# Optimization experiments

Measured on AMD Instinct MI355X. Metric: run time of the kernel, lower is better.

## Reference

```python
import jax, jax.numpy as jnp
import numpy as np

B, G, A, C = 32, 2704, 3, 6
D, H, W = 1024, 52, 52
L, HID, K = 20, 512, 128


def setup_inputs() -> dict:
    key = jax.random.key(0)
    ks = jax.random.split(key, 7)
    return {
        "boxes": jax.random.normal(ks[0], (B, G, A, C), dtype=jnp.float32),
        "feature": jax.random.normal(ks[1], (B, D, H, W), dtype=jnp.float32),
        "text": jax.random.normal(ks[2], (B, L, HID), dtype=jnp.float32),
        "W_vs": jax.random.normal(ks[3], (D, HID), dtype=jnp.float32) * 0.02,
        "b_vs": jax.random.normal(ks[4], (HID,), dtype=jnp.float32) * 0.02,
        "W_tx": jax.random.normal(ks[5], (HID, HID), dtype=jnp.float32) * 0.02,
        "b_tx": jax.random.normal(ks[6], (HID,), dtype=jnp.float32) * 0.02,
        "select_num": K,
    }


def reference(boxes, feature, text, W_vs, b_vs, W_tx, b_tx, select_num):
    # objectness score: mean over anchors, channel 4  -> [B, G]
    score = jnp.mean(boxes, axis=2)[:, :, 4]
    _, idx = jax.lax.top_k(score, select_num)          # [B, K]
    # torch path builds a boolean mask then masked_select, which keeps
    # selected cells in grid order -> sort indices ascending
    idx = jnp.sort(idx, axis=1)

    # gather selected boxes: [B, K, A, C]
    sel_boxes = jnp.take_along_axis(boxes, idx[:, :, None, None], axis=1)

    b, d, h, w = feature.shape
    feat = feature.reshape(b, d, h * w).transpose(0, 2, 1)  # [B, G, D]
    sel_feat = jnp.take_along_axis(feat, idx[:, :, None], axis=1)  # [B, K, D]

    linear_feature = sel_feat @ W_vs + b_vs   # [B, K, HID]
    linear_text = text @ W_tx + b_tx          # [B, L, HID]

    # pack head inputs into a single array for baseline comparison
    out = jnp.concatenate([linear_feature, linear_text], axis=1)  # [B, K+L, HID]
    return out, sel_boxes
```

## Files before the change

kernel.cpp:

```cpp
#include <hip/hip_runtime.h>
#include <cstddef>

namespace {
constexpr int cB = 32;
constexpr int cG = 2704;
constexpr int cA = 3;
constexpr int cC = 6;
constexpr int cD = 1024;
constexpr int cL = 20;
constexpr int cH = 512;
constexpr int cK = 128;
constexpr int ROWS_OUT = cK + cL;
constexpr int FTHREADS = 512;
constexpr int CHUNK = (cG + FTHREADS - 1) / FTHREADS;
}

using u16x8 = __attribute__((ext_vector_type(8))) unsigned short;
using f32x4 = __attribute__((ext_vector_type(4))) float;
using bf16x8 = __attribute__((ext_vector_type(8))) short;

static __device__ __forceinline__ unsigned short f2bf(float f) {
  unsigned u = __float_as_uint(f);
  unsigned rounding = 0x7fffu + ((u >> 16) & 1u);
  return (unsigned short)((u + rounding) >> 16);
}
static __device__ __forceinline__ unsigned packbf(float lo, float hi) {
  return (unsigned)f2bf(lo) | ((unsigned)f2bf(hi) << 16);
}

__global__ __launch_bounds__(FTHREADS) void front_kernel(
    const float* __restrict__ boxes, const float* __restrict__ W_vs,
    const float* __restrict__ W_tx, const float* __restrict__ text,
    int* __restrict__ idx_out, float* __restrict__ out_boxes,
    unsigned short* __restrict__ Wt_vs, unsigned short* __restrict__ Wt_tx,
    unsigned short* __restrict__ text_bf) {
  __shared__ unsigned su[cG];
  __shared__ int hist[256];
  __shared__ int wsum[8];
  __shared__ int ssel[cK];
  __shared__ int s_rem;
  __shared__ unsigned s_prefix;
  __shared__ float tile[64][65];

  const int tid = threadIdx.x;
  const int lane = tid & 63;
  const int wv = tid >> 6;

  if (blockIdx.x < cB) {
    const int b = blockIdx.x;
    for (int g = tid; g < cG; g += FTHREADS) {
      const float* p = boxes + ((size_t)(b * cG + g) * cA) * cC + 4;
      float s = (p[0] + p[cC] + p[2 * cC]) * (1.0f / 3.0f);
      unsigned bits = __float_as_uint(s);
      su[g] = (bits & 0x80000000u) ? ~bits : (bits | 0x80000000u);
    }
    __syncthreads();

    int remaining = cK;
    unsigned prefix = 0;
    for (int pass = 0; pass < 4; ++pass) {
      const int shift = 24 - 8 * pass;
      if (tid < 256) hist[tid] = 0;
      __syncthreads();
      for (int g = tid; g < cG; g += FTHREADS) {
        unsigned u = su[g];
        if ((pass == 0) || ((u >> (shift + 8)) == (prefix >> (shift + 8))))
          atomicAdd(&hist[(u >> shift) & 255], 1);
      }
      __syncthreads();
      if (tid < 256) {
        int h = hist[tid];
        int x = h;
#pragma unroll
        for (int d = 1; d < 64; d <<= 1) {
          int n = __shfl_up(x, d);
          if (lane >= d) x += n;
        }
        if (lane == 63) wsum[wv] = x;
        __syncthreads();
        int off = 0, T = 0;
#pragma unroll
        for (int w = 0; w < 4; ++w) {
          int s = wsum[w];
          T += s;
          if (w < wv) off += s;
        }
        const int pincl = x + off;
        const int pexcl = pincl - h;
        const int target = T - remaining;
        if (target >= pexcl && target < pincl) {
          s_prefix = prefix | ((unsigned)tid << shift);
          s_rem = remaining - (T - pincl);
        }
      } else {
        __syncthreads();
      }
      __syncthreads();
      remaining = s_rem;
      prefix = s_prefix;
    }

    const int g0 = tid * CHUNK;
    const int g1 = min(g0 + CHUNK, cG);
    int cgt = 0, ceq = 0;
    for (int g = g0; g < g1; ++g) {
      unsigned u = su[g];
      cgt += (u > prefix);
      ceq += (u == prefix);
    }
    int packed = (cgt << 16) | ceq;
    int x = packed;
#pragma unroll
    for (int d = 1; d < 64; d <<= 1) {
      int n = __shfl_up(x, d);
      if (lane >= d) x += n;
    }
    if (lane == 63) wsum[wv] = x;
    __syncthreads();
    int off = 0;
#pragma unroll
    for (int w = 0; w < 8; ++w)
      if (w < wv) off += wsum[w];
    const int excl = x + off - packed;
    int gt_before = excl >> 16;
    int eq_before = excl & 0xffff;

    for (int g = g0; g < g1; ++g) {
      unsigned u = su[g];
      if (u > prefix) {
        ssel[gt_before + min(eq_before, remaining)] = g;
        ++gt_before;
      } else if (u == prefix) {
        if (eq_before < remaining) ssel[gt_before + eq_before] = g;
        ++eq_before;
      }
    }
    __syncthreads();

    if (tid < cK) idx_out[b * cK + tid] = ssel[tid];
    for (int t2 = tid; t2 < cK * (cA * cC); t2 += FTHREADS) {
      const int k = t2 / 18;
      const int e = t2 - k * 18;
      out_boxes[(size_t)(b * cK + k) * 18 + e] =
          boxes[((size_t)(b * cG) + ssel[k]) * 18 + e];
    }
  } else {
    const int t = blockIdx.x - cB;
    if (t < 128) {
      const int k0 = (t >> 3) * 64, n0 = (t & 7) * 64;
      for (int i = tid; i < 1024; i += FTHREADS) {
        const int kk = i >> 4, c4 = (i & 15) * 4;
        const float4 v =
            *(const float4*)(W_vs + (size_t)(k0 + kk) * cH + n0 + c4);
        tile[kk][c4 + 0] = v.x;
        tile[kk][c4 + 1] = v.y;
        tile[kk][c4 + 2] = v.z;
        tile[kk][c4 + 3] = v.w;
      }
      __syncthreads();
      for (int j = tid; j < 2048; j += FTHREADS) {
        const int nn = j >> 5, p = j & 31;
        unsigned v = packbf(tile[2 * p][nn], tile[2 * p + 1][nn]);
        *(unsigned*)(Wt_vs + (size_t)(n0 + nn) * cD + k0 + 2 * p) = v;
      }
    } else if (t < 192) {
      const int t2 = t - 128;
      const int k0 = (t2 >> 3) * 64, n0 = (t2 & 7) * 64;
      for (int i = tid; i < 1024; i += FTHREADS) {
        const int kk = i >> 4, c4 = (i & 15) * 4;
        const float4 v =
            *(const float4*)(W_tx + (size_t)(k0 + kk) * cH + n0 + c4);
        tile[kk][c4 + 0] = v.x;
        tile[kk][c4 + 1] = v.y;
        tile[kk][c4 + 2] = v.z;
        tile[kk][c4 + 3] = v.w;
      }
      __syncthreads();
      for (int j = tid; j < 2048; j += FTHREADS) {
        const int nn = j >> 5, p = j & 31;
        unsigned v = packbf(tile[2 * p][nn], tile[2 * p + 1][nn]);
        *(unsigned*)(Wt_tx + (size_t)(n0 + nn) * cH + k0 + 2 * p) = v;
      }
    } else {
      const int t3 = t - 192;
      const size_t base = (size_t)t3 * 4096;
      for (int i = tid; i < 1024; i += FTHREADS) {
        const float4 v = *(const float4*)(text + base + (size_t)i * 4);
        uint2 pv;
        pv.x = packbf(v.x, v.y);
        pv.y = packbf(v.z, v.w);
        *(uint2*)(text_bf + base + (size_t)i * 4) = pv;
      }
    }
  }
}

__global__ __launch_bounds__(256) void gather_feat_kernel(
    const float* __restrict__ feature, const int* __restrict__ idx,
    unsigned short* __restrict__ selfeat) {
  const int kc = blockIdx.x;
  const int dc = blockIdx.y;
  const int b = blockIdx.z;
  const int tid = threadIdx.x;
  const int lane = tid & 63;
  const int grp = tid >> 6;
  __shared__ int sidx[64];
  __shared__ float tile[32][65];
  if (tid < 64) sidx[tid] = idx[b * cK + kc * 64 + tid];
  __syncthreads();

  const int g = sidx[lane];
  const float* fptr =
      feature + (size_t)b * cD * cG + (size_t)(dc * 32 + grp * 8) * cG + g;
  float f[8];
#pragma unroll
  for (int j = 0; j < 8; ++j) f[j] = __builtin_nontemporal_load(fptr + (size_t)j * cG);
#pragma unroll
  for (int j = 0; j < 8; ++j) tile[grp * 8 + j][lane] = f[j];
  __syncthreads();

  const size_t obase = ((size_t)(b * cK + kc * 64)) * cD + dc * 32;
#pragma unroll
  for (int it = 0; it < 2; ++it) {
    const int i = tid + it * 256;
    const int kk = i >> 3;
    const int q = i & 7;
    uint2 pv;
    pv.x = packbf(tile[4 * q + 0][kk], tile[4 * q + 1][kk]);
    pv.y = packbf(tile[4 * q + 2][kk], tile[4 * q + 3][kk]);
    *(uint2*)(selfeat + obase + (size_t)kk * cD + 4 * q) = pv;
  }
}

template <int KD>
__device__ __forceinline__ void mfma_gemm_body(
    const unsigned short* __restrict__ A, const unsigned short* __restrict__ Bt,
    const float* __restrict__ bias, float* __restrict__ out, int bm, int bn,
    int rpb, int row_off, unsigned short (*As)[128][40],
    unsigned short (*Bs)[128][40]) {
  constexpr int NT = KD / 32;
  const int tid = threadIdx.x;
  const int wid = tid >> 6, lane = tid & 63;
  const int wr = wid >> 2, wc = wid & 3;
  const int lr = lane & 15, lg = lane >> 4;

  const int srow = tid >> 2;
  const int sc = (tid & 3) * 8;

  const unsigned short* pA = A + (size_t)(bm * 128 + srow) * KD + sc;
  const unsigned short* pB = Bt + (size_t)(bn * 128 + srow) * KD + sc;

  f32x4 acc[4][2];
#pragma unroll
  for (int i = 0; i < 4; ++i)
#pragma unroll
    for (int j = 0; j < 2; ++j) acc[i][j] = {0.f, 0.f, 0.f, 0.f};

  u16x8 xa, xb;
  u16x8 ya, yb;

#define LOAD_X(kt)                      \
  xa = *(const u16x8*)(pA + (kt) * 32); \
  xb = *(const u16x8*)(pB + (kt) * 32);
#define LOAD_Y(kt)                      \
  ya = *(const u16x8*)(pA + (kt) * 32); \
  yb = *(const u16x8*)(pB + (kt) * 32);
#define STORE_X(buf)                \
  *(u16x8*)&As[buf][srow][sc] = xa; \
  *(u16x8*)&Bs[buf][srow][sc] = xb;
#define STORE_Y(buf)                \
  *(u16x8*)&As[buf][srow][sc] = ya; \
  *(u16x8*)&Bs[buf][srow][sc] = yb;
#define COMPUTE(buf)                                                        \
  {                                                                         \
    bf16x8 af[4], bfr[2];                                                   \
    _Pragma("unroll") for (int fr = 0; fr < 4; ++fr) af[fr] =               \
        *(const bf16x8*)&As[buf][wr * 64 + fr * 16 + lr][lg * 8];           \
    _Pragma("unroll") for (int fc = 0; fc < 2; ++fc) bfr[fc] =              \
        *(const bf16x8*)&Bs[buf][wc * 32 + fc * 16 + lr][lg * 8];           \
    _Pragma("unroll") for (int fr = 0; fr < 4; ++fr)                        \
        _Pragma("unroll") for (int fc = 0; fc < 2; ++fc) acc[fr][fc] =      \
            __builtin_amdgcn_mfma_f32_16x16x32_bf16(af[fr], bfr[fc],        \
                                                    acc[fr][fc], 0, 0, 0);  \
  }

  LOAD_X(0);
  LOAD_Y(1);
  STORE_X(0);
  __syncthreads();

  for (int t = 0; t < NT; t += 2) {
    if (t + 2 < NT) LOAD_X(t + 2);
    COMPUTE(0);
    STORE_Y(1);
    __syncthreads();
    if (t + 3 < NT) LOAD_Y(t + 3);
    COMPUTE(1);
    if (t + 2 < NT) STORE_X(0);
    __syncthreads();
  }
#undef LOAD_X
#undef LOAD_Y
#undef STORE_X
#undef STORE_Y
#undef COMPUTE

  float biasv[2];
#pragma unroll
  for (int fc = 0; fc < 2; ++fc)
    biasv[fc] = bias[bn * 128 + wc * 32 + fc * 16 + lr];

#pragma unroll
  for (int fr = 0; fr < 4; ++fr) {
#pragma unroll
    for (int fc = 0; fc < 2; ++fc) {
      const int col = bn * 128 + wc * 32 + fc * 16 + lr;
#pragma unroll
      for (int j = 0; j < 4; ++j) {
        const int row = bm * 128 + wr * 64 + fr * 16 + lg * 4 + j;
        const int bb = row / rpb;
        const int rr = row - bb * rpb;
        out[(size_t)bb * (ROWS_OUT * cH) + (size_t)(row_off + rr) * cH + col] =
            acc[fr][fc][j] + biasv[fc];
      }
    }
  }
}

__global__ __launch_bounds__(512) void gemms_kernel(
    const unsigned short* __restrict__ selfeat,
    const unsigned short* __restrict__ Wt_vs,
    const unsigned short* __restrict__ text_bf,
    const unsigned short* __restrict__ Wt_tx, const float* __restrict__ b_vs,
    const float* __restrict__ b_tx, float* __restrict__ out) {
  __shared__ unsigned short As[2][128][40];
  __shared__ unsigned short Bs[2][128][40];
  const int blk = blockIdx.x;
  if (blk < 128) {
    const int w = ((blk & 7) << 4) | (blk >> 3);
    mfma_gemm_body<1024>(selfeat, Wt_vs, b_vs, out, w >> 2, w & 3, 128, 0, As,
                         Bs);
  } else {
    const int t = blk - 128;
    mfma_gemm_body<512>(text_bf, Wt_tx, b_tx, out, t >> 2, t & 3, cL, cK, As,
                        Bs);
  }
}

extern "C" void kernel_launch(void* const* d_in, const int* in_sizes, int n_in,
                              void* d_out, int out_size, void* d_ws,
                              size_t ws_size, hipStream_t stream) {
  const float* boxes = (const float*)d_in[0];
  const float* feature = (const float*)d_in[1];
  const float* text = (const float*)d_in[2];
  const float* W_vs = (const float*)d_in[3];
  const float* b_vs = (const float*)d_in[4];
  const float* W_tx = (const float*)d_in[5];
  const float* b_tx = (const float*)d_in[6];

  float* out = (float*)d_out;
  float* out_boxes = out + (size_t)cB * ROWS_OUT * cH;

  int* idx = (int*)d_ws;
  unsigned short* selfeat = (unsigned short*)((char*)d_ws + 16384);
  unsigned short* Wt_vs = (unsigned short*)((char*)d_ws + 8404992);
  unsigned short* Wt_tx = (unsigned short*)((char*)d_ws + 9453568);
  unsigned short* text_bf = (unsigned short*)((char*)d_ws + 9977856);

  front_kernel<<<cB + 272, FTHREADS, 0, stream>>>(
      boxes, W_vs, W_tx, text, idx, out_boxes, Wt_vs, Wt_tx, text_bf);

  {
    dim3 grid(2, 32, 32);
    gather_feat_kernel<<<grid, 256, 0, stream>>>(feature, idx, selfeat);
  }

  gemms_kernel<<<148, 512, 0, stream>>>(selfeat, Wt_vs, text_bf, Wt_tx, b_vs,
                                        b_tx, out);
}
```

Baseline: 81.04 us.

## Merge feature gather with text GEMM and split vision GEMM into own kernel

The feature gather and the small text GEMM now share one launch, so the text GEMM blocks can run alongside gather blocks instead of waiting behind the whole gather. The vision GEMM gets its own kernel that depends only on the gathered features. Gather blocks grow from 256 to 512 threads, each covering 64 feature channels, and reuse the GEMM shared-memory buffers for their tile. Nontemporal loads are swapped for plain loads. The number of launches stays the same, but the gather's occupancy and cache behaviour change.

```diff
diff --git a/kernel.cpp b/kernel.cpp
--- a/kernel.cpp
+++ b/kernel.cpp
@@ -192,43 +192,6 @@
         *(uint2*)(text_bf + base + (size_t)i * 4) = pv;
       }
     }
-  }
-}
-
-__global__ __launch_bounds__(256) void gather_feat_kernel(
-    const float* __restrict__ feature, const int* __restrict__ idx,
-    unsigned short* __restrict__ selfeat) {
-  const int kc = blockIdx.x;
-  const int dc = blockIdx.y;
-  const int b = blockIdx.z;
-  const int tid = threadIdx.x;
-  const int lane = tid & 63;
-  const int grp = tid >> 6;
-  __shared__ int sidx[64];
-  __shared__ float tile[32][65];
-  if (tid < 64) sidx[tid] = idx[b * cK + kc * 64 + tid];
-  __syncthreads();
-
-  const int g = sidx[lane];
-  const float* fptr =
-      feature + (size_t)b * cD * cG + (size_t)(dc * 32 + grp * 8) * cG + g;
-  float f[8];
-#pragma unroll
-  for (int j = 0; j < 8; ++j) f[j] = __builtin_nontemporal_load(fptr + (size_t)j * cG);
-#pragma unroll
-  for (int j = 0; j < 8; ++j) tile[grp * 8 + j][lane] = f[j];
-  __syncthreads();
-
-  const size_t obase = ((size_t)(b * cK + kc * 64)) * cD + dc * 32;
-#pragma unroll
-  for (int it = 0; it < 2; ++it) {
-    const int i = tid + it * 256;
-    const int kk = i >> 3;
-    const int q = i & 7;
-    uint2 pv;
-    pv.x = packbf(tile[4 * q + 0][kk], tile[4 * q + 1][kk]);
-    pv.y = packbf(tile[4 * q + 2][kk], tile[4 * q + 3][kk]);
-    *(uint2*)(selfeat + obase + (size_t)kk * cD + 4 * q) = pv;
   }
 }
 
@@ -327,24 +290,66 @@
   }
 }
 
-__global__ __launch_bounds__(512) void gemms_kernel(
-    const unsigned short* __restrict__ selfeat,
-    const unsigned short* __restrict__ Wt_vs,
+__global__ __launch_bounds__(512) void mid_kernel(
+    const float* __restrict__ feature, const int* __restrict__ idx,
+    unsigned short* __restrict__ selfeat,
     const unsigned short* __restrict__ text_bf,
-    const unsigned short* __restrict__ Wt_tx, const float* __restrict__ b_vs,
-    const float* __restrict__ b_tx, float* __restrict__ out) {
-  __shared__ unsigned short As[2][128][40];
-  __shared__ unsigned short Bs[2][128][40];
+    const unsigned short* __restrict__ Wt_tx, const float* __restrict__ b_tx,
+    float* __restrict__ out) {
+  __shared__ __align__(16) unsigned short As[2][128][40];
+  __shared__ __align__(16) unsigned short Bs[2][128][40];
   const int blk = blockIdx.x;
-  if (blk < 128) {
-    const int w = ((blk & 7) << 4) | (blk >> 3);
-    mfma_gemm_body<1024>(selfeat, Wt_vs, b_vs, out, w >> 2, w & 3, 128, 0, As,
-                         Bs);
+  const int tid = threadIdx.x;
+
+  if (blk < 1024) {
+    const int kc = blk & 1;
+    const int dc = (blk >> 1) & 15;
+    const int b = blk >> 5;
+    const int lane = tid & 63;
+    const int grp = tid >> 6;
+    int* sidx = (int*)&Bs[0][0][0];
+    float(*tile)[65] = (float(*)[65]) & As[0][0][0];
+
+    if (tid < 64) sidx[tid] = idx[b * cK + kc * 64 + tid];
+    __syncthreads();
+
+    const int g = sidx[lane];
+    const float* fptr =
+        feature + (size_t)b * cD * cG + (size_t)(dc * 64 + grp * 8) * cG + g;
+    float f[8];
+#pragma unroll
+    for (int j = 0; j < 8; ++j) f[j] = fptr[(size_t)j * cG];
+#pragma unroll
+    for (int j = 0; j < 8; ++j) tile[grp * 8 + j][lane] = f[j];
+    __syncthreads();
+
+    const size_t obase = ((size_t)(b * cK + kc * 64)) * cD + dc * 64;
+#pragma unroll
+    for (int it = 0; it < 2; ++it) {
+      const int i = tid + it * 512;
+      const int kk = i >> 4;
+      const int q = i & 15;
+      uint2 pv;
+      pv.x = packbf(tile[4 * q + 0][kk], tile[4 * q + 1][kk]);
+      pv.y = packbf(tile[4 * q + 2][kk], tile[4 * q + 3][kk]);
+      *(uint2*)(selfeat + obase + (size_t)kk * cD + 4 * q) = pv;
+    }
   } else {
-    const int t = blk - 128;
+    const int t = blk - 1024;
     mfma_gemm_body<512>(text_bf, Wt_tx, b_tx, out, t >> 2, t & 3, cL, cK, As,
                         Bs);
   }
+}
+
+__global__ __launch_bounds__(512) void gemm1_kernel(
+    const unsigned short* __restrict__ selfeat,
+    const unsigned short* __restrict__ Wt_vs, const float* __restrict__ b_vs,
+    float* __restrict__ out) {
+  __shared__ __align__(16) unsigned short As[2][128][40];
+  __shared__ __align__(16) unsigned short Bs[2][128][40];
+  const int w = ((blockIdx.x & 7) << 4) | (blockIdx.x >> 3);
+  mfma_gemm_body<1024>(selfeat, Wt_vs, b_vs, out, w >> 2, w & 3, 128, 0, As,
+                       Bs);
 }
 
 extern "C" void kernel_launch(void* const* d_in, const int* in_sizes, int n_in,
@@ -370,11 +375,8 @@
   front_kernel<<<cB + 272, FTHREADS, 0, stream>>>(
       boxes, W_vs, W_tx, text, idx, out_boxes, Wt_vs, Wt_tx, text_bf);
 
-  {
-    dim3 grid(2, 32, 32);
-    gather_feat_kernel<<<grid, 256, 0, stream>>>(feature, idx, selfeat);
-  }
-
-  gemms_kernel<<<148, 512, 0, stream>>>(selfeat, Wt_vs, text_bf, Wt_tx, b_vs,
-                                        b_tx, out);
-}
+  mid_kernel<<<1044, 512, 0, stream>>>(feature, idx, selfeat, text_bf, Wt_tx,
+                                       b_tx, out);
+
+  gemm1_kernel<<<128, 512, 0, stream>>>(selfeat, Wt_vs, b_vs, out);
+}
```

Measured after the change: 82.43 us. About the same (+1.7%).
